# Optimization experiments

Measured on AMD Instinct MI355X. Metric: run time of the kernel, lower is better.

Reference implementation:

```python
import jax, jax.numpy as jnp
import numpy as np

EPS = 1e-7
B, F, C, H, W, D = 2, 2, 64, 32, 104, 96


def _pix_homog(h, w):
    ys, xs = jnp.meshgrid(jnp.arange(h, dtype=jnp.float32),
                          jnp.arange(w, dtype=jnp.float32), indexing='ij')
    return jnp.stack([xs.ravel(), ys.ravel(), jnp.ones(h * w, jnp.float32)], 0)  # [3, H*W]


def setup_inputs() -> dict:
    key = jax.random.key(0)
    k1, k2 = jax.random.split(key)
    current_feats = jax.random.normal(k1, (B, C, H, W), jnp.float32)
    lookup_feats = jax.random.normal(k2, (B, F, C, H, W), jnp.float32)

    rng = np.random.RandomState(0)
    # intrinsics at matching (feature) resolution, monodepth2-style
    Km = np.eye(4, dtype=np.float32)
    Km[0, 0] = 0.58 * W
    Km[1, 1] = 1.92 * H
    Km[0, 2] = 0.5 * W
    Km[1, 2] = 0.5 * H
    K = np.tile(Km[None], (B, 1, 1))
    invK = np.linalg.inv(K).astype(np.float32)

    # near-identity relative poses (small rotation perturbation + small translation)
    poses = np.tile(np.eye(4, dtype=np.float32)[None, None], (B, F, 1, 1))
    poses[:, :, :3, :3] += 0.02 * rng.randn(B, F, 3, 3).astype(np.float32)
    poses[:, :, :3, 3] = 0.1 * rng.randn(B, F, 3).astype(np.float32)

    depth_bins = jnp.linspace(0.1, 20.0, D, dtype=jnp.float32)
    return {
        'current_feats': current_feats,
        'lookup_feats': lookup_feats,
        'poses': jnp.asarray(poses),
        'K': jnp.asarray(K),
        'invK': jnp.asarray(invK),
        'depth_bins': depth_bins,
    }


def _grid_sample_zeros(lfT, gx, gy, h, w):
    """Bilinear grid_sample, align_corners=True, padding_mode='zeros'.
    lfT: [B,F,H,W,C]; gx,gy: [B,F,D,H,W] in pixel coords. -> [B,F,D,H,W,C]"""
    x0 = jnp.floor(gx)
    y0 = jnp.floor(gy)
    x0i = x0.astype(jnp.int32)
    y0i = y0.astype(jnp.int32)
    wx1 = gx - x0
    wy1 = gy - y0
    wx0 = 1.0 - wx1
    wy0 = 1.0 - wy1
    bb = jnp.arange(lfT.shape[0])[:, None, None, None, None]
    ff = jnp.arange(lfT.shape[1])[None, :, None, None, None]

    def corner(yi, xi, wgt):
        m = ((xi >= 0) & (xi < w) & (yi >= 0) & (yi < h)).astype(lfT.dtype)
        xc = jnp.clip(xi, 0, w - 1)
        yc = jnp.clip(yi, 0, h - 1)
        v = lfT[bb, ff, yc, xc]                      # [B,F,D,H,W,C]
        return v * (m * wgt)[..., None]

    return (corner(y0i, x0i, wy0 * wx0) + corner(y0i, x0i + 1, wy0 * wx1)
            + corner(y0i + 1, x0i, wy1 * wx0) + corner(y0i + 1, x0i + 1, wy1 * wx1))


def reference(current_feats, lookup_feats, poses, K, invK, depth_bins):
    b, c, h, w = current_feats.shape
    f = lookup_feats.shape[1]
    d = depth_bins.shape[0]

    # Backproject: world points for each hypothesised depth plane
    pix = _pix_homog(h, w)                                   # [3, HW]
    cam = jnp.einsum('bij,jn->bin', invK[:, :3, :3], pix)    # [B,3,HW]
    pts = depth_bins[None, :, None, None] * cam[:, None]     # [B,D,3,HW]
    world = jnp.concatenate([pts, jnp.ones((b, d, 1, h * w), pts.dtype)], 2)  # [B,D,4,HW]

    # Project into each lookup frame
    P = jnp.einsum('bij,bfjk->bfik', K, poses)[:, :, :3, :]  # [B,F,3,4]
    cpts = jnp.einsum('bfij,bdjn->bfdin', P, world)          # [B,F,D,3,HW]
    xy = cpts[:, :, :, :2] / (cpts[:, :, :, 2:3] + EPS)      # pixel coords [B,F,D,2,HW]
    xy = xy.reshape(b, f, d, 2, h, w)
    gx, gy = xy[:, :, :, 0], xy[:, :, :, 1]                  # [B,F,D,H,W]

    # edge mask (detach in original -> stop_gradient)
    sx, sy = jax.lax.stop_gradient(gx), jax.lax.stop_gradient(gy)
    edge = ((sx >= 2.0) & (sx <= w - 2) & (sy >= 2.0) & (sy <= h - 2)).astype(jnp.float32)
    interior = jnp.zeros((h, w), jnp.float32).at[2:-2, 2:-2].set(1.0)
    edge_mask = edge * interior                               # [B,F,D,H,W]

    # warp lookup features and L1-diff against current features
    lfT = lookup_feats.transpose(0, 1, 3, 4, 2)               # [B,F,H,W,C]
    warped = _grid_sample_zeros(lfT, gx, gy, h, w)            # [B,F,D,H,W,C]
    cur = current_feats.transpose(0, 2, 3, 1)                 # [B,H,W,C]
    diffs = jnp.abs(warped - cur[:, None, None]).mean(-1) * edge_mask  # [B,F,D,H,W]

    # skip lookup frames whose pose is all-zero
    valid = (poses.sum((-2, -1)) != 0).astype(jnp.float32)    # [B,F]
    diffs = diffs * valid[:, :, None, None, None]

    cost = diffs.sum(1)                                        # [B,D,H,W]
    counts = (diffs > 0).astype(jnp.float32).sum(1)
    cost = cost / (counts + EPS)

    # set missing values to per-pixel max over depth bins
    missing = (cost == 0.0)
    cmax = cost.max(1, keepdims=True)
    cost = jnp.where(missing, cmax, cost)
    return cost
```

## Files before the change

### kernel.cpp

```cpp
#include <hip/hip_runtime.h>
#include <math.h>

constexpr int B_ = 2, F_ = 2, C_ = 64, H_ = 32, W_ = 104, D_ = 96;
constexpr int HW_ = H_ * W_;
#define EPSF 1e-7f

constexpr size_t LFT_ELEMS  = (size_t)B_ * F_ * HW_ * C_;
constexpr size_t CURT_OFF_F = LFT_ELEMS / 2;

constexpr int NT_BLKS = (HW_ / 32) * (C_ / 32) * (B_ * F_ + B_);
constexpr int PXB   = 4;
constexpr int XT_   = W_ / PXB;
constexpr int DPAD  = D_ + 1;
constexpr int DPADI = D_ + 4;


template<int CTRL>
__device__ __forceinline__ float dpp_add(float x) {
    int y = __builtin_amdgcn_update_dpp(0, __float_as_int(x), CTRL, 0xf, 0xf, true);
    return x + __int_as_float(y);
}
__device__ __forceinline__ float group16_sum(float s) {
    s = dpp_add<0xB1>(s);
    s = dpp_add<0x4E>(s);
    s = dpp_add<0x141>(s);
    s = dpp_add<0x140>(s);
    return s;
}

__device__ __forceinline__ ushort f2bf(float f) {
    unsigned u = __float_as_uint(f);
    u += 0x7FFFu + ((u >> 16) & 1u);
    return (ushort)(u >> 16);
}

__device__ __forceinline__ float dot2bf(unsigned a, unsigned b, float acc) {
    float r;
    asm("v_dot2_f32_bf16 %0, %1, %2, %3" : "=v"(r) : "v"(a), "v"(b), "v"(acc));
    return r;
}

__global__ __launch_bounds__(256) void prep_kernel(
        const float* __restrict__ cur, const float* __restrict__ lf,
        float* __restrict__ ws) {
    __shared__ float tile[32][33];
    int bid = blockIdx.x;
    int slice = bid / 208;
    int rem   = bid % 208;
    int nb = rem % 104, cb = rem / 104;
    const float* inS = (slice < B_ * F_)
        ? lf  + (size_t)slice * C_ * HW_
        : cur + (size_t)(slice - B_ * F_) * C_ * HW_;
    int t = threadIdx.x;
    int tx = t & 31, ty = t >> 5;
    int n0 = nb * 32, c0 = cb * 32;
    #pragma unroll
    for (int k = 0; k < 32; k += 8)
        tile[ty + k][tx] = inS[(size_t)(c0 + ty + k) * HW_ + n0 + tx];
    __syncthreads();
    if (slice < B_ * F_) {
        ushort* outS = (ushort*)ws + (size_t)slice * HW_ * C_;
        #pragma unroll
        for (int k = 0; k < 32; k += 8)
            outS[(size_t)(n0 + ty + k) * C_ + c0 + tx] = f2bf(tile[tx][ty + k]);
    } else {
        float* outS = ws + CURT_OFF_F + (size_t)(slice - B_ * F_) * HW_ * C_;
        #pragma unroll
        for (int k = 0; k < 32; k += 8)
            outS[(size_t)(n0 + ty + k) * C_ + c0 + tx] = tile[tx][ty + k];
    }
}

__global__ __launch_bounds__(256, 4) void mega_kernel(
        const float* __restrict__ poses, const float* __restrict__ K,
        const float* __restrict__ invK, const float* __restrict__ depth_bins,
        const float* __restrict__ ws, float* __restrict__ out) {
    int t   = threadIdx.x;
    int bid = blockIdx.x;
    int xt  = bid % XT_;  int r = bid / XT_;
    int y   = r % H_;
    int b   = r / H_;

    if (y < 2 || y >= H_ - 2) {
        for (int k = t; k < PXB * D_; k += 256) {
            int d = k >> 2, px = k & 3;
            out[((size_t)(b * D_ + d) * H_ + y) * W_ + xt * PXB + px] = 0.0f;
        }
        return;
    }

    __shared__ alignas(16) int offsL[F_][PXB][DPADI];
    __shared__ alignas(16) uint2 wtsL[F_][PXB][DPAD];
    __shared__ float  costb[PXB][DPAD];
    __shared__ float  pmax[32][PXB];
    __shared__ float  cmaxb[PXB];

    {
        int pxA = t & 3;
        int xA  = xt * PXB + pxA;
        const float* iK = invK + (size_t)b * 16;
        float xf = (float)xA, yf = (float)y;
        float cam0 = __fmul_rn(iK[0], xf); cam0 = __fmaf_rn(iK[1], yf, cam0); cam0 = __fmaf_rn(iK[2],  1.0f, cam0);
        float cam1 = __fmul_rn(iK[4], xf); cam1 = __fmaf_rn(iK[5], yf, cam1); cam1 = __fmaf_rn(iK[6],  1.0f, cam1);
        float cam2 = __fmul_rn(iK[8], xf); cam2 = __fmaf_rn(iK[9], yf, cam2); cam2 = __fmaf_rn(iK[10], 1.0f, cam2);
        bool interior = (xA >= 2) && (xA <= W_ - 3);

        #pragma unroll
        for (int f = 0; f < F_; ++f) {
            const float* Kb   = K + (size_t)b * 16;
            const float* pose = poses + (size_t)(b * F_ + f) * 16;
            float P[12];
            #pragma unroll
            for (int i = 0; i < 3; ++i) {
                #pragma unroll
                for (int k = 0; k < 4; ++k) {
                    float acc = __fmul_rn(Kb[i*4+0], pose[0*4+k]);
                    acc = __fmaf_rn(Kb[i*4+1], pose[1*4+k], acc);
                    acc = __fmaf_rn(Kb[i*4+2], pose[2*4+k], acc);
                    acc = __fmaf_rn(Kb[i*4+3], pose[3*4+k], acc);
                    P[i*4+k] = acc;
                }
            }
            float vs = 0.f;
            #pragma unroll
            for (int j = 0; j < 16; ++j) vs += pose[j];
            bool valid = (vs != 0.f);

            #pragma unroll
            for (int k = 0; k < 2; ++k) {
                int idx = t + 256 * k;
                if (idx < PXB * D_) {
                    int dd = idx >> 2;
                    float depth = depth_bins[dd];
                    float p0 = __fmul_rn(depth, cam0);
                    float p1 = __fmul_rn(depth, cam1);
                    float p2 = __fmul_rn(depth, cam2);
                    float c0 = __fmul_rn(P[0], p0); c0 = __fmaf_rn(P[1], p1, c0); c0 = __fmaf_rn(P[2],  p2, c0); c0 = __fmaf_rn(P[3],  1.0f, c0);
                    float c1 = __fmul_rn(P[4], p0); c1 = __fmaf_rn(P[5], p1, c1); c1 = __fmaf_rn(P[6],  p2, c1); c1 = __fmaf_rn(P[7],  1.0f, c1);
                    float c2 = __fmul_rn(P[8], p0); c2 = __fmaf_rn(P[9], p1, c2); c2 = __fmaf_rn(P[10], p2, c2); c2 = __fmaf_rn(P[11], 1.0f, c2);
                    float denom = __fadd_rn(c2, EPSF);
                    float gx = c0 / denom;
                    float gy = c1 / denom;
                    bool m = valid && interior && (gx >= 2.0f) && (gx <= (float)(W_ - 2))
                                               && (gy >= 2.0f) && (gy <= (float)(H_ - 2));
                    if (m) {
                        float x0f = floorf(gx), y0f = floorf(gy);
                        int   x0  = (int)x0f,   y0  = (int)y0f;
                        float wx1 = gx - x0f, wy1 = gy - y0f;
                        float wx0 = 1.f - wx1, wy0 = 1.f - wy1;
                        unsigned wlo = ((unsigned)f2bf(wy0 * wx1) << 16) | f2bf(wy0 * wx0);
                        unsigned whi = ((unsigned)f2bf(wy1 * wx1) << 16) | f2bf(wy1 * wx0);
                        wtsL[f][pxA][dd] = make_uint2(wlo, whi);
                        offsL[f][pxA][dd] = (y0 * W_ + x0) * C_;
                    } else {
                        offsL[f][pxA][dd] = -1;
                        wtsL[f][pxA][dd] = make_uint2(0u, 0u);
                    }
                }
            }
        }
    }
    __syncthreads();

    {
        int lane = t & 15, px = (t >> 4) & 3, half = t >> 6;
        int x = xt * PXB + px;
        const float4 cv = *(const float4*)(ws + CURT_OFF_F
                            + ((size_t)((b * H_ + y) * W_ + x)) * C_ + lane * 4);
        const ushort* lfbase = (const ushort*)ws;
        const ushort* lf0a = lfbase + (size_t)(b * F_ + 0) * HW_ * C_ + lane * 4;
        const ushort* lf0b = lf0a + W_ * C_;
        const ushort* lf1a = lfbase + (size_t)(b * F_ + 1) * HW_ * C_ + lane * 4;
        const ushort* lf1b = lf1a + W_ * C_;

        int dbeg = half * (D_ / 4);
        for (int ki4 = 0; ki4 < D_ / 16; ++ki4) {
            int dc4 = dbeg + ki4 * 4;
            int4 oq0 = *(const int4*)&offsL[0][px][dc4];
            int4 oq1 = *(const int4*)&offsL[1][px][dc4];
            int oa0[4] = {oq0.x, oq0.y, oq0.z, oq0.w};
            int oa1[4] = {oq1.x, oq1.y, oq1.z, oq1.w};

            #pragma unroll
            for (int jp = 0; jp < 2; ++jp) {
                uint2 q[2][8];
                #pragma unroll
                for (int u = 0; u < 2; ++u) {
                    int j = jp * 2 + u;
                    int oc0 = oa0[j], oc1 = oa1[j];
                    int os0 = oc0 & ~(oc0 >> 31);
                    int os1 = oc1 & ~(oc1 >> 31);
                    q[u][0] = *(const uint2*)(lf0a + os0);
                    q[u][1] = *(const uint2*)(lf0a + os0 + C_);
                    q[u][2] = *(const uint2*)(lf0b + os0);
                    q[u][3] = *(const uint2*)(lf0b + os0 + C_);
                    q[u][4] = *(const uint2*)(lf1a + os1);
                    q[u][5] = *(const uint2*)(lf1a + os1 + C_);
                    q[u][6] = *(const uint2*)(lf1b + os1);
                    q[u][7] = *(const uint2*)(lf1b + os1 + C_);
                }
                #pragma unroll
                for (int u = 0; u < 2; ++u) {
                    int j = jp * 2 + u;
                    int dc = dc4 + j;
                    uint2 w0 = wtsL[0][px][dc], w1 = wtsL[1][px][dc];
                    bool m0 = (oa0[j] >= 0), m1 = (oa1[j] >= 0);

                    float costsum = 0.f, counts = 0.f;
                    {
                        unsigned a0 = __builtin_amdgcn_perm(q[u][0].x, q[u][1].x, 0x01000504u);
                        unsigned a1 = __builtin_amdgcn_perm(q[u][0].x, q[u][1].x, 0x03020706u);
                        unsigned a2 = __builtin_amdgcn_perm(q[u][0].y, q[u][1].y, 0x01000504u);
                        unsigned a3 = __builtin_amdgcn_perm(q[u][0].y, q[u][1].y, 0x03020706u);
                        unsigned b0 = __builtin_amdgcn_perm(q[u][2].x, q[u][3].x, 0x01000504u);
                        unsigned b1 = __builtin_amdgcn_perm(q[u][2].x, q[u][3].x, 0x03020706u);
                        unsigned b2 = __builtin_amdgcn_perm(q[u][2].y, q[u][3].y, 0x01000504u);
                        unsigned b3 = __builtin_amdgcn_perm(q[u][2].y, q[u][3].y, 0x03020706u);
                        float s0 = dot2bf(b0, w0.y, dot2bf(a0, w0.x, -cv.x));
                        float s1 = dot2bf(b1, w0.y, dot2bf(a1, w0.x, -cv.y));
                        float s2 = dot2bf(b2, w0.y, dot2bf(a2, w0.x, -cv.z));
                        float s3 = dot2bf(b3, w0.y, dot2bf(a3, w0.x, -cv.w));
                        float s = (fabsf(s0) + fabsf(s1)) + (fabsf(s2) + fabsf(s3));
                        s = group16_sum(s);
                        float diff = __fmul_rn(s, 1.0f / 64.0f) * (m0 ? 1.0f : 0.0f);
                        costsum += diff;
                        counts  += (diff > 0.f) ? 1.0f : 0.0f;
                    }
                    {
                        unsigned a0 = __builtin_amdgcn_perm(q[u][4].x, q[u][5].x, 0x01000504u);
                        unsigned a1 = __builtin_amdgcn_perm(q[u][4].x, q[u][5].x, 0x03020706u);
                        unsigned a2 = __builtin_amdgcn_perm(q[u][4].y, q[u][5].y, 0x01000504u);
                        unsigned a3 = __builtin_amdgcn_perm(q[u][4].y, q[u][5].y, 0x03020706u);
                        unsigned b0 = __builtin_amdgcn_perm(q[u][6].x, q[u][7].x, 0x01000504u);
                        unsigned b1 = __builtin_amdgcn_perm(q[u][6].x, q[u][7].x, 0x03020706u);
                        unsigned b2 = __builtin_amdgcn_perm(q[u][6].y, q[u][7].y, 0x01000504u);
                        unsigned b3 = __builtin_amdgcn_perm(q[u][6].y, q[u][7].y, 0x03020706u);
                        float s0 = dot2bf(b0, w1.y, dot2bf(a0, w1.x, -cv.x));
                        float s1 = dot2bf(b1, w1.y, dot2bf(a1, w1.x, -cv.y));
                        float s2 = dot2bf(b2, w1.y, dot2bf(a2, w1.x, -cv.z));
                        float s3 = dot2bf(b3, w1.y, dot2bf(a3, w1.x, -cv.w));
                        float s = (fabsf(s0) + fabsf(s1)) + (fabsf(s2) + fabsf(s3));
                        s = group16_sum(s);
                        float diff = __fmul_rn(s, 1.0f / 64.0f) * (m1 ? 1.0f : 0.0f);
                        costsum += diff;
                        counts  += (diff > 0.f) ? 1.0f : 0.0f;
                    }
                    float cost = costsum * __builtin_amdgcn_rcpf(__fadd_rn(counts, EPSF));
                    if (lane == 0) costb[px][dc] = cost;
                }
            }
        }
    }
    __syncthreads();

    {
        int j = t >> 2, px = t & 3;
        float v[3];
        if (t < 128) {
            float pm = 0.f;
            #pragma unroll
            for (int k = 0; k < 3; ++k) {
                v[k] = costb[px][j + 32 * k];
                pm = fmaxf(pm, v[k]);
            }
            pmax[j][px] = pm;
        }
        __syncthreads();
        if (t < PXB) {
            float cm = 0.f;
            #pragma unroll
            for (int jj = 0; jj < 32; ++jj) cm = fmaxf(cm, pmax[jj][t]);
            cmaxb[t] = cm;
        }
        __syncthreads();
        if (t < 128) {
            float cm = cmaxb[px];
            int x = xt * PXB + px;
            #pragma unroll
            for (int k = 0; k < 3; ++k) {
                int d = j + 32 * k;
                out[((size_t)(b * D_ + d) * H_ + y) * W_ + x] = (v[k] == 0.0f) ? cm : v[k];
            }
        }
    }
}

extern "C" void kernel_launch(void* const* d_in, const int* in_sizes, int n_in,
                              void* d_out, int out_size, void* d_ws, size_t ws_size,
                              hipStream_t stream) {
    const float* cur        = (const float*)d_in[0];
    const float* lf         = (const float*)d_in[1];
    const float* poses      = (const float*)d_in[2];
    const float* K          = (const float*)d_in[3];
    const float* invK       = (const float*)d_in[4];
    const float* depth_bins = (const float*)d_in[5];
    float* out = (float*)d_out;
    float* ws  = (float*)d_ws;

    prep_kernel<<<NT_BLKS, 256, 0, stream>>>(cur, lf, ws);
    mega_kernel<<<B_ * H_ * XT_, 256, 0, stream>>>(poses, K, invK, depth_bins, ws, out);
}
```

Baseline: 105.6 us.

## Pre-pack horizontally adjacent bf16 pixel pairs to drop perms and halve gather loads

The prep kernel now stores lookup features as 32-bit words, each holding the bf16 values of pixel n and pixel n+1 for one channel. It loads an extra halo column into the transpose tile so the pair at the tile edge is complete. The main kernel then fetches each bilinear row pair with one 16-byte load instead of two 8-byte loads, and feeds the words straight into dot2 with no byte-permute instructions. In exchange the lookup-feature workspace doubles, so there is more prep write traffic and cache footprint, and the host-side workspace allocation must be large enough for the new offset of the current features.

After: 96.39 us. 8.8% less time.

```diff
diff --git a/kernel.cpp b/kernel.cpp
--- a/kernel.cpp
+++ b/kernel.cpp
@@ -5,8 +5,8 @@
 constexpr int HW_ = H_ * W_;
 #define EPSF 1e-7f
 
-constexpr size_t LFT_ELEMS  = (size_t)B_ * F_ * HW_ * C_;
-constexpr size_t CURT_OFF_F = LFT_ELEMS / 2;
+constexpr size_t LFP_ELEMS  = (size_t)B_ * F_ * HW_ * C_;
+constexpr size_t CURT_OFF_F = LFP_ELEMS;
 
 constexpr int NT_BLKS = (HW_ / 32) * (C_ / 32) * (B_ * F_ + B_);
 constexpr int PXB   = 4;
@@ -54,15 +54,22 @@
     int t = threadIdx.x;
     int tx = t & 31, ty = t >> 5;
     int n0 = nb * 32, c0 = cb * 32;
+    int nx = (n0 + 32 < HW_) ? (n0 + 32) : (HW_ - 1);
     #pragma unroll
-    for (int k = 0; k < 32; k += 8)
+    for (int k = 0; k < 32; k += 8) {
         tile[ty + k][tx] = inS[(size_t)(c0 + ty + k) * HW_ + n0 + tx];
+        if (tx == 0)
+            tile[ty + k][32] = inS[(size_t)(c0 + ty + k) * HW_ + nx];
+    }
     __syncthreads();
     if (slice < B_ * F_) {
-        ushort* outS = (ushort*)ws + (size_t)slice * HW_ * C_;
+        unsigned* outS = (unsigned*)ws + (size_t)slice * HW_ * C_;
         #pragma unroll
-        for (int k = 0; k < 32; k += 8)
-            outS[(size_t)(n0 + ty + k) * C_ + c0 + tx] = f2bf(tile[tx][ty + k]);
+        for (int k = 0; k < 32; k += 8) {
+            unsigned lo = f2bf(tile[tx][ty + k]);
+            unsigned hi = f2bf(tile[tx][ty + k + 1]);
+            outS[(size_t)(n0 + ty + k) * C_ + c0 + tx] = lo | (hi << 16);
+        }
     } else {
         float* outS = ws + CURT_OFF_F + (size_t)(slice - B_ * F_) * HW_ * C_;
         #pragma unroll
@@ -167,11 +174,11 @@
         int x = xt * PXB + px;
         const float4 cv = *(const float4*)(ws + CURT_OFF_F
                             + ((size_t)((b * H_ + y) * W_ + x)) * C_ + lane * 4);
-        const ushort* lfbase = (const ushort*)ws;
-        const ushort* lf0a = lfbase + (size_t)(b * F_ + 0) * HW_ * C_ + lane * 4;
-        const ushort* lf0b = lf0a + W_ * C_;
-        const ushort* lf1a = lfbase + (size_t)(b * F_ + 1) * HW_ * C_ + lane * 4;
-        const ushort* lf1b = lf1a + W_ * C_;
+        const unsigned* pfbase = (const unsigned*)ws;
+        const unsigned* pf0a = pfbase + (size_t)(b * F_ + 0) * HW_ * C_ + lane * 4;
+        const unsigned* pf0b = pf0a + W_ * C_;
+        const unsigned* pf1a = pfbase + (size_t)(b * F_ + 1) * HW_ * C_ + lane * 4;
+        const unsigned* pf1b = pf1a + W_ * C_;
 
         int dbeg = half * (D_ / 4);
         for (int ki4 = 0; ki4 < D_ / 16; ++ki4) {
@@ -183,21 +190,17 @@
 
             #pragma unroll
             for (int jp = 0; jp < 2; ++jp) {
-                uint2 q[2][8];
+                uint4 q[2][4];
                 #pragma unroll
                 for (int u = 0; u < 2; ++u) {
                     int j = jp * 2 + u;
                     int oc0 = oa0[j], oc1 = oa1[j];
                     int os0 = oc0 & ~(oc0 >> 31);
                     int os1 = oc1 & ~(oc1 >> 31);
-                    q[u][0] = *(const uint2*)(lf0a + os0);
-                    q[u][1] = *(const uint2*)(lf0a + os0 + C_);
-                    q[u][2] = *(const uint2*)(lf0b + os0);
-                    q[u][3] = *(const uint2*)(lf0b + os0 + C_);
-                    q[u][4] = *(const uint2*)(lf1a + os1);
-                    q[u][5] = *(const uint2*)(lf1a + os1 + C_);
-                    q[u][6] = *(const uint2*)(lf1b + os1);
-                    q[u][7] = *(const uint2*)(lf1b + os1 + C_);
+                    q[u][0] = *(const uint4*)(pf0a + os0);
+                    q[u][1] = *(const uint4*)(pf0b + os0);
+                    q[u][2] = *(const uint4*)(pf1a + os1);
+                    q[u][3] = *(const uint4*)(pf1b + os1);
                 }
                 #pragma unroll
                 for (int u = 0; u < 2; ++u) {
@@ -205,21 +208,15 @@
                     int dc = dc4 + j;
                     uint2 w0 = wtsL[0][px][dc], w1 = wtsL[1][px][dc];
                     bool m0 = (oa0[j] >= 0), m1 = (oa1[j] >= 0);
+                    uint4 A0 = q[u][0], B0 = q[u][1];
+                    uint4 A1 = q[u][2], B1 = q[u][3];
 
                     float costsum = 0.f, counts = 0.f;
                     {
-                        unsigned a0 = __builtin_amdgcn_perm(q[u][0].x, q[u][1].x, 0x01000504u);
-                        unsigned a1 = __builtin_amdgcn_perm(q[u][0].x, q[u][1].x, 0x03020706u);
-                        unsigned a2 = __builtin_amdgcn_perm(q[u][0].y, q[u][1].y, 0x01000504u);
-                        unsigned a3 = __builtin_amdgcn_perm(q[u][0].y, q[u][1].y, 0x03020706u);
-                        unsigned b0 = __builtin_amdgcn_perm(q[u][2].x, q[u][3].x, 0x01000504u);
-                        unsigned b1 = __builtin_amdgcn_perm(q[u][2].x, q[u][3].x, 0x03020706u);
-                        unsigned b2 = __builtin_amdgcn_perm(q[u][2].y, q[u][3].y, 0x01000504u);
-                        unsigned b3 = __builtin_amdgcn_perm(q[u][2].y, q[u][3].y, 0x03020706u);
-                        float s0 = dot2bf(b0, w0.y, dot2bf(a0, w0.x, -cv.x));
-                        float s1 = dot2bf(b1, w0.y, dot2bf(a1, w0.x, -cv.y));
-                        float s2 = dot2bf(b2, w0.y, dot2bf(a2, w0.x, -cv.z));
-                        float s3 = dot2bf(b3, w0.y, dot2bf(a3, w0.x, -cv.w));
+                        float s0 = dot2bf(B0.x, w0.y, dot2bf(A0.x, w0.x, -cv.x));
+                        float s1 = dot2bf(B0.y, w0.y, dot2bf(A0.y, w0.x, -cv.y));
+                        float s2 = dot2bf(B0.z, w0.y, dot2bf(A0.z, w0.x, -cv.z));
+                        float s3 = dot2bf(B0.w, w0.y, dot2bf(A0.w, w0.x, -cv.w));
                         float s = (fabsf(s0) + fabsf(s1)) + (fabsf(s2) + fabsf(s3));
                         s = group16_sum(s);
                         float diff = __fmul_rn(s, 1.0f / 64.0f) * (m0 ? 1.0f : 0.0f);
@@ -227,18 +224,10 @@
                         counts  += (diff > 0.f) ? 1.0f : 0.0f;
                     }
                     {
-                        unsigned a0 = __builtin_amdgcn_perm(q[u][4].x, q[u][5].x, 0x01000504u);
-                        unsigned a1 = __builtin_amdgcn_perm(q[u][4].x, q[u][5].x, 0x03020706u);
-                        unsigned a2 = __builtin_amdgcn_perm(q[u][4].y, q[u][5].y, 0x01000504u);
-                        unsigned a3 = __builtin_amdgcn_perm(q[u][4].y, q[u][5].y, 0x03020706u);
-                        unsigned b0 = __builtin_amdgcn_perm(q[u][6].x, q[u][7].x, 0x01000504u);
-                        unsigned b1 = __builtin_amdgcn_perm(q[u][6].x, q[u][7].x, 0x03020706u);
-                        unsigned b2 = __builtin_amdgcn_perm(q[u][6].y, q[u][7].y, 0x01000504u);
-                        unsigned b3 = __builtin_amdgcn_perm(q[u][6].y, q[u][7].y, 0x03020706u);
-                        float s0 = dot2bf(b0, w1.y, dot2bf(a0, w1.x, -cv.x));
-                        float s1 = dot2bf(b1, w1.y, dot2bf(a1, w1.x, -cv.y));
-                        float s2 = dot2bf(b2, w1.y, dot2bf(a2, w1.x, -cv.z));
-                        float s3 = dot2bf(b3, w1.y, dot2bf(a3, w1.x, -cv.w));
+                        float s0 = dot2bf(B1.x, w1.y, dot2bf(A1.x, w1.x, -cv.x));
+                        float s1 = dot2bf(B1.y, w1.y, dot2bf(A1.y, w1.x, -cv.y));
+                        float s2 = dot2bf(B1.z, w1.y, dot2bf(A1.z, w1.x, -cv.z));
+                        float s3 = dot2bf(B1.w, w1.y, dot2bf(A1.w, w1.x, -cv.w));
                         float s = (fabsf(s0) + fabsf(s1)) + (fabsf(s2) + fabsf(s3));
                         s = group16_sum(s);
                         float diff = __fmul_rn(s, 1.0f / 64.0f) * (m1 ? 1.0f : 0.0f);
```
